# Performance work log

Hardware: AMD Instinct MI355X
Metric: run time of the kernel (lower is better)

## Reference

```python
import jax, jax.numpy as jnp
import numpy as np

C = 256
LN_EPS = 1e-5
LEAKY_SLOPE = 0.01

def _layernorm(t, g, b):
    mu = jnp.mean(t, axis=-1, keepdims=True)
    var = jnp.mean((t - mu) ** 2, axis=-1, keepdims=True)
    return (t - mu) * jax.lax.rsqrt(var + LN_EPS) * g + b

def setup_inputs() -> dict:
    key = jax.random.key(0)
    ks = jax.random.split(key, 16)
    b, d, h, w = 4, 4096, 64, 64
    s = lambda n: 1.0 / np.sqrt(n)
    return {
        "x": jax.random.normal(ks[0], (b, 1, d), jnp.float32),
        "y": jax.random.normal(ks[1], (b, C, h, w), jnp.float32),
        "q_w": jax.random.normal(ks[2], (C, C), jnp.float32) * s(C),
        "q_b": jnp.zeros((C,), jnp.float32),
        "dw_w": jax.random.normal(ks[3], (C,), jnp.float32),
        "dw_b": jnp.zeros((C,), jnp.float32),
        "kv_w1": jax.random.normal(ks[4], (1, C // 2), jnp.float32),
        "kv_b1": jnp.zeros((C // 2,), jnp.float32),
        "ln1_g": jnp.ones((C // 2,), jnp.float32),
        "ln1_b": jnp.zeros((C // 2,), jnp.float32),
        "kv_w2": jax.random.normal(ks[5], (C // 2, C), jnp.float32) * s(C // 2),
        "kv_b2": jnp.zeros((C,), jnp.float32),
        "ln2_g": jnp.ones((C,), jnp.float32),
        "ln2_b": jnp.zeros((C,), jnp.float32),
        "kv_w3": jax.random.normal(ks[6], (C, C), jnp.float32) * s(C),
        "kv_b3": jnp.zeros((C,), jnp.float32),
        "ln3_g": jnp.ones((C,), jnp.float32),
        "ln3_b": jnp.zeros((C,), jnp.float32),
        "kv_w4": jax.random.normal(ks[7], (C, 2 * C), jnp.float32) * s(C),
        "kv_b4": jnp.zeros((2 * C,), jnp.float32),
        "proj_w": jax.random.normal(ks[8], (C, C), jnp.float32) * s(C),
        "proj_b": jnp.zeros((C,), jnp.float32),
    }

def reference(x, y, q_w, q_b, dw_w, dw_b, kv_w1, kv_b1, ln1_g, ln1_b,
              kv_w2, kv_b2, ln2_g, ln2_b, kv_w3, kv_b3, ln3_g, ln3_b,
              kv_w4, kv_b4, proj_w, proj_b):
    b, c, h, w = y.shape
    # x: [b, 1, d] -> [b, d, 1]; MLP kv-generator lifts each scalar to 2c channels
    t = jnp.swapaxes(x, 1, 2)  # [b, d, 1]
    t = jax.nn.leaky_relu(_layernorm(t @ kv_w1 + kv_b1, ln1_g, ln1_b), LEAKY_SLOPE)
    t = jax.nn.leaky_relu(_layernorm(t @ kv_w2 + kv_b2, ln2_g, ln2_b), LEAKY_SLOPE)
    t = jax.nn.leaky_relu(_layernorm(t @ kv_w3 + kv_b3, ln3_g, ln3_b), LEAKY_SLOPE)
    t = jax.nn.silu(t @ kv_w4 + kv_b4)  # [b, d, 2c]
    k, v = jnp.split(t, 2, axis=-1)  # each [b, d, c]
    k = jnp.swapaxes(k, 1, 2)  # [b, c, d]
    # q = dwconv1x1(conv1x1(y)): 1x1 conv is a channel matmul; depthwise 1x1 is per-channel affine
    q = jnp.einsum('bchw,oc->bohw', y, q_w) + q_b[None, :, None, None]
    q = q * dw_w[None, :, None, None] + dw_b[None, :, None, None]
    q = q.reshape(b, c, h * w).transpose(0, 2, 1)  # [b, hw, c]
    scores = jnp.einsum('bic,bcd->bid', q, k) * (float(c) ** -0.5)  # [b, hw, d]
    attn = jax.nn.softmax(scores, axis=2)
    h_ = jnp.einsum('bid,bdc->bic', attn, v)  # [b, hw, c]
    h_ = h_.transpose(0, 2, 1).reshape(b, c, h, w)
    h_ = jnp.einsum('bchw,oc->bohw', h_, proj_w) + proj_b[None, :, None, None]
    return y + h_
```

## Files before the change

kernel.cpp:

```cpp
#include <hip/hip_runtime.h>
#include <cstdint>
#include <cstddef>

using bf16   = __bf16;
using bf16x8 = __bf16 __attribute__((ext_vector_type(8)));
using f32x4  = float  __attribute__((ext_vector_type(4)));
using u16    = unsigned short;
using ushort8 = __attribute__((ext_vector_type(8))) unsigned short;

#define MFMA16(a, b, c) __builtin_amdgcn_mfma_f32_16x16x32_bf16(a, b, c, 0, 0, 0)

__device__ __forceinline__ u16 f2bf(float f) {
  union { float f; unsigned u; } v; v.f = f;
  unsigned r = v.u + 0x7fffu + ((v.u >> 16) & 1u);
  return (u16)(r >> 16);
}
__device__ __forceinline__ u16 bfc(float f) {
  union { float f; unsigned u; } v; v.f = f;
  return (u16)((v.u + 0x8000u) >> 16);
}
__device__ __forceinline__ float b2f(u16 h) {
  union { unsigned u; float f; } v; v.u = ((unsigned)h) << 16; return v.f;
}
__device__ __forceinline__ bf16x8 ldb8(const u16* p) { return *(const bf16x8*)p; }
__device__ __forceinline__ float red_sum16(float v) {
  v += __shfl_xor(v, 1, 64); v += __shfl_xor(v, 2, 64);
  v += __shfl_xor(v, 4, 64); v += __shfl_xor(v, 8, 64);
  return v;
}
__device__ __forceinline__ void gll16(const u16* g, u16* l) {
  __builtin_amdgcn_global_load_lds(
      (const __attribute__((address_space(1))) void*)g,
      (__attribute__((address_space(3))) void*)l, 16, 0, 0);
}

#define QSCALE 0.09016844005556021f

__global__ void k_prep(const float* __restrict__ kv_w2, const float* __restrict__ kv_w3,
                       const float* __restrict__ kv_w4, const float* __restrict__ q_w,
                       const float* __restrict__ proj_w,
                       u16* __restrict__ Wt2, u16* __restrict__ Wt3, u16* __restrict__ Wt4,
                       u16* __restrict__ Qw, u16* __restrict__ Pww) {
  int idx = blockIdx.x * 256 + threadIdx.x;
  if (idx < 32768) {
    int n = idx >> 7, k = idx & 127;
    Wt2[idx] = f2bf(kv_w2[k * 256 + n]);
  } else if (idx < 98304) {
    int j = idx - 32768, n = j >> 8, k = j & 255;
    Wt3[j] = f2bf(kv_w3[k * 256 + n]);
  } else if (idx < 229376) {
    int j = idx - 98304, n = j >> 8, k = j & 255;
    Wt4[j] = f2bf(kv_w4[k * 512 + n]);
  } else if (idx < 294912) {
    int j = idx - 229376;
    Qw[j] = f2bf(q_w[j]);
  } else if (idx < 360448) {
    int j = idx - 294912;
    Pww[j] = f2bf(proj_w[j]);
  }
}

__device__ __forceinline__ void ln_store(f32x4* acc, const float* __restrict__ bias,
    const float* __restrict__ g, const float* __restrict__ bb, u16* act,
    int w, int quad, int l16) {
  #pragma unroll
  for (int f = 0; f < 16; ++f) {
    float bv = bias[f * 16 + l16];
    acc[f][0] += bv; acc[f][1] += bv; acc[f][2] += bv; acc[f][3] += bv;
  }
  #pragma unroll
  for (int r = 0; r < 4; ++r) {
    float s = 0;
    #pragma unroll
    for (int f = 0; f < 16; ++f) s += acc[f][r];
    s = red_sum16(s);
    float mu = s * (1.f / 256.f);
    float vv = 0;
    #pragma unroll
    for (int f = 0; f < 16; ++f) { float d = acc[f][r] - mu; vv += d * d; }
    vv = red_sum16(vv);
    float inv = rsqrtf(vv * (1.f / 256.f) + 1e-5f);
    int rl = w * 16 + quad * 4 + r;
    #pragma unroll
    for (int f = 0; f < 16; ++f) {
      int col = f * 16 + l16;
      float o = (acc[f][r] - mu) * inv * g[col] + bb[col];
      o = o > 0.f ? o : 0.01f * o;
      act[rl * 264 + col] = f2bf(o);
    }
  }
}

template<int K>
__device__ __forceinline__ void mlp_layer(u16* act, u16* sW, const u16* __restrict__ Wt,
    const float* __restrict__ bias, const float* __restrict__ g, const float* __restrict__ bb,
    int tid, int w, int quad, int l16) {
  bf16x8 af[K / 32];
  #pragma unroll
  for (int kk = 0; kk < K / 32; ++kk) af[kk] = ldb8(act + (w * 16 + l16) * 264 + kk * 32 + quad * 8);
  f32x4 z = {0.f, 0.f, 0.f, 0.f};
  f32x4 acc[16];
  #pragma unroll
  for (int f = 0; f < 16; ++f) acc[f] = z;
  for (int nc = 0; nc < 8; ++nc) {
    __syncthreads();
    #pragma unroll
    for (int p = 0; p < K / 64; ++p) {
      int q = p * 256 + tid; int row = q / (K / 8), c8 = q % (K / 8);
      *(uint4*)(sW + row * 264 + c8 * 8) = *(const uint4*)(Wt + (size_t)(nc * 32 + row) * K + c8 * 8);
    }
    __syncthreads();
    #pragma unroll
    for (int nb = 0; nb < 2; ++nb) {
      int f = nc * 2 + nb;
      #pragma unroll
      for (int kk = 0; kk < K / 32; ++kk)
        acc[f] = MFMA16(af[kk], ldb8(sW + (nb * 16 + l16) * 264 + kk * 32 + quad * 8), acc[f]);
    }
  }
  ln_store(acc, bias, g, bb, act, w, quad, l16);
  __syncthreads();
}

__device__ __forceinline__ void mlp_layer4(u16* act, u16* sW, const u16* __restrict__ Wt4,
    const float* __restrict__ bias4, u16* __restrict__ Kt, u16* __restrict__ Vt,
    int i0, int tid, int w, int quad, int l16) {
  bf16x8 af[8];
  #pragma unroll
  for (int kk = 0; kk < 8; ++kk) af[kk] = ldb8(act + (w * 16 + l16) * 264 + kk * 32 + quad * 8);
  f32x4 z = {0.f, 0.f, 0.f, 0.f};
  for (int h = 0; h < 2; ++h) {
    f32x4 acc[16];
    #pragma unroll
    for (int f = 0; f < 16; ++f) acc[f] = z;
    for (int nc = 0; nc < 8; ++nc) {
      __syncthreads();
      #pragma unroll
      for (int p = 0; p < 4; ++p) {
        int q = p * 256 + tid; int row = q >> 5, c8 = q & 31;
        *(uint4*)(sW + row * 264 + c8 * 8) =
            *(const uint4*)(Wt4 + (size_t)(h * 256 + nc * 32 + row) * 256 + c8 * 8);
      }
      __syncthreads();
      #pragma unroll
      for (int nb = 0; nb < 2; ++nb) {
        int f = nc * 2 + nb;
        #pragma unroll
        for (int kk = 0; kk < 8; ++kk)
          acc[f] = MFMA16(af[kk], ldb8(sW + (nb * 16 + l16) * 264 + kk * 32 + quad * 8), acc[f]);
      }
    }
    #pragma unroll
    for (int f = 0; f < 16; ++f) {
      int col = f * 16 + l16;
      float bv = bias4[h * 256 + col];
      if (h == 0) {
        int kk = f >> 1;
        int qs = (f & 1) * 2 + (l16 >> 3);
        int e  = l16 & 7;
        int l16base = (w & 1) * 8 + quad * 2;
        size_t tb = ((size_t)((i0 >> 5) + (w >> 1))) * 8192 + kk * 1024 + qs * 128 + e;
        #pragma unroll
        for (int r = 0; r < 4; ++r) {
          float v = acc[f][r] + bv;
          v = v / (1.f + __expf(-v));
          Kt[tb + (size_t)(r & 1) * 512 + (size_t)(l16base + (r >> 1)) * 8] = f2bf(v);
        }
      } else {
        int rowg0 = i0 + w * 16 + quad * 4;
        int bb2 = rowg0 >> 12;
        int tt = (rowg0 >> 5) & 127;
        int qv = (rowg0 >> 3) & 3;
        int e0 = rowg0 & 7;
        ushort4 u;
        #pragma unroll
        for (int r = 0; r < 4; ++r) {
          float v = acc[f][r] + bv;
          v = v / (1.f + __expf(-v));
          ((u16*)&u)[r] = f2bf(v);
        }
        size_t off = ((size_t)(bb2 * 128 + tt)) * 8192 + f * 512 + qv * 128 + l16 * 8 + e0;
        *(ushort4*)(Vt + off) = u;
      }
    }
  }
}

__global__ __launch_bounds__(256, 2) void k_fused(
    const float* __restrict__ x, const float* __restrict__ w1, const float* __restrict__ bias1,
    const float* __restrict__ g1, const float* __restrict__ bb1,
    const u16* __restrict__ Wt2, const float* __restrict__ bias2,
    const float* __restrict__ g2, const float* __restrict__ bb2,
    const u16* __restrict__ Wt3, const float* __restrict__ bias3,
    const float* __restrict__ g3, const float* __restrict__ bb3,
    const u16* __restrict__ Wt4, const float* __restrict__ bias4,
    const float* __restrict__ y, const u16* __restrict__ Qw,
    const float* __restrict__ qb, const float* __restrict__ dww, const float* __restrict__ dwb,
    u16* __restrict__ Kt, u16* __restrict__ Vt, u16* __restrict__ Qb) {
  __shared__ __align__(16) u16 smem[25344];
  int tid = threadIdx.x, w = tid >> 6, lane = tid & 63, quad = lane >> 4, l16 = lane & 15;

  if (blockIdx.x < 256) {
    u16* act = smem;
    u16* sW  = smem + 16896;
    int i0 = blockIdx.x * 64;
    {
      int rloc = w * 16 + (lane >> 2);
      int c0 = (lane & 3) * 32;
      float xv = x[i0 + rloc];
      float t[32];
      float s = 0.f;
      #pragma unroll
      for (int j = 0; j < 32; ++j) { t[j] = xv * w1[c0 + j] + bias1[c0 + j]; s += t[j]; }
      s += __shfl_xor(s, 1, 64); s += __shfl_xor(s, 2, 64);
      float mu = s * (1.f / 128.f);
      float vv = 0.f;
      #pragma unroll
      for (int j = 0; j < 32; ++j) { float d = t[j] - mu; vv += d * d; }
      vv += __shfl_xor(vv, 1, 64); vv += __shfl_xor(vv, 2, 64);
      float inv = rsqrtf(vv * (1.f / 128.f) + 1e-5f);
      #pragma unroll
      for (int jo = 0; jo < 4; ++jo) {
        ushort8 pk;
        #pragma unroll
        for (int e = 0; e < 8; ++e) {
          int j = jo * 8 + e;
          float o = (t[j] - mu) * inv * g1[c0 + j] + bb1[c0 + j];
          o = o > 0.f ? o : 0.01f * o;
          pk[e] = f2bf(o);
        }
        *(ushort8*)(act + rloc * 264 + c0 + jo * 8) = pk;
      }
    }
    __syncthreads();
    mlp_layer<128>(act, sW, Wt2, bias2, g2, bb2, tid, w, quad, l16);
    mlp_layer<256>(act, sW, Wt3, bias3, g3, bb3, tid, w, quad, l16);
    mlp_layer4(act, sW, Wt4, bias4, Kt, Vt, i0, tid, w, quad, l16);
    return;
  }

  u16* sY = smem;
  u16* sB = smem + 4608;
  int t = blockIdx.x - 256;
  int b = t >> 6, i0 = (t & 63) * 64;
  f32x4 z = {0.f, 0.f, 0.f, 0.f};
  f32x4 acc[16];
  #pragma unroll
  for (int f = 0; f < 16; ++f) acc[f] = z;
  for (int kc = 0; kc < 4; ++kc) {
    if (kc) __syncthreads();
    {
      int cl = tid >> 4;
      int il = (tid & 15) * 4;
      #pragma unroll
      for (int p = 0; p < 4; ++p) {
        int c = kc * 64 + p * 16 + cl;
        float4 v = *(const float4*)(y + ((size_t)(b * 256 + c)) * 4096 + i0 + il);
        sY[(il + 0) * 72 + p * 16 + cl] = f2bf(v.x);
        sY[(il + 1) * 72 + p * 16 + cl] = f2bf(v.y);
        sY[(il + 2) * 72 + p * 16 + cl] = f2bf(v.z);
        sY[(il + 3) * 72 + p * 16 + cl] = f2bf(v.w);
      }
    }
    #pragma unroll
    for (int p = 0; p < 8; ++p) {
      int q = p * 256 + tid; int row = q >> 3, k8 = q & 7;
      *(uint4*)(sB + row * 72 + k8 * 8) = *(const uint4*)(Qw + (size_t)row * 256 + kc * 64 + k8 * 8);
    }
    __syncthreads();
    #pragma unroll
    for (int kk = 0; kk < 2; ++kk) {
      bf16x8 af = ldb8(sY + (w * 16 + l16) * 72 + kk * 32 + quad * 8);
      #pragma unroll
      for (int f = 0; f < 16; ++f) {
        bf16x8 bfr = ldb8(sB + (f * 16 + l16) * 72 + kk * 32 + quad * 8);
        acc[f] = MFMA16(af, bfr, acc[f]);
      }
    }
  }
  #pragma unroll
  for (int f = 0; f < 16; ++f) {
    int col = f * 16 + l16;
    float q0 = qb[col], sc = dww[col], dB = dwb[col];
    #pragma unroll
    for (int r = 0; r < 4; ++r) {
      int rowg = i0 + w * 16 + quad * 4 + r;
      float v = ((acc[f][r] + q0) * sc + dB) * QSCALE;
      Qb[((size_t)(b * 4096 + rowg)) * 256 + col] = f2bf(v);
    }
  }
}

__global__ __launch_bounds__(256, 2) void k_attn(const u16* __restrict__ Qb, const u16* __restrict__ Kt,
    const u16* __restrict__ Vt, u16* __restrict__ Op, float* __restrict__ Ol) {
  __shared__ __align__(16) u16 smem[37888];
  int tid = threadIdx.x, w = tid >> 6, lane = tid & 63, quad = lane >> 4, l16 = lane & 15;
  int b = blockIdx.x & 3, kh = (blockIdx.x >> 2) & 3, qt = blockIdx.x >> 4;
  int i0 = qt * 128 + w * 32;

  bf16x8 qf[2][8];
  {
    const u16* qrow = Qb + ((size_t)(b * 4096 + i0 + l16)) * 256 + quad * 8;
    #pragma unroll
    for (int kk = 0; kk < 8; ++kk) {
      qf[0][kk] = ldb8(qrow + kk * 32);
      qf[1][kk] = ldb8(qrow + 16 * 256 + kk * 32);
    }
  }
  f32x4 z = {0.f, 0.f, 0.f, 0.f};
  f32x4 oacc[2][16];
  #pragma unroll
  for (int sub = 0; sub < 2; ++sub)
    #pragma unroll
    for (int f = 0; f < 16; ++f) oacc[sub][f] = z;
  float l4[2][4] = {{0.f, 0.f, 0.f, 0.f}, {0.f, 0.f, 0.f, 0.f}};

  u16* sPw = smem + 32768 + w * 1280;
  int wp = w & 1;
  const u16* gSrc = ((w < 2) ? Kt : Vt) + ((size_t)(b * 128 + kh * 32) * 8192) + wp * 4096 + lane * 8;
  u16* lBase = smem + ((w < 2) ? 0 : 8192) + wp * 4096 + lane * 8;

  #pragma unroll
  for (int i = 0; i < 8; ++i) gll16(gSrc + i * 512, lBase + i * 512);
  gSrc += 8192;

  #pragma unroll 1
  for (int kt = 0; kt < 32; ++kt) {
    int buf = kt & 1;
    const u16* sK = smem + buf * 16384;
    const u16* sV = sK + 8192;
    asm volatile("s_waitcnt vmcnt(0)" ::: "memory");
    __syncthreads();
    if (kt < 31) {
      u16* dst = lBase + (buf ^ 1) * 16384;
      #pragma unroll
      for (int i = 0; i < 8; ++i) gll16(gSrc + i * 512, dst + i * 512);
      gSrc += 8192;
    }
    f32x4 s00 = z, s01 = z, s10 = z, s11 = z;
    const u16* kb = sK + lane * 8;
    __builtin_amdgcn_s_setprio(1);
    #pragma unroll
    for (int kk = 0; kk < 8; ++kk) {
      bf16x8 k0 = ldb8(kb + kk * 1024);
      bf16x8 k1 = ldb8(kb + kk * 1024 + 512);
      s00 = MFMA16(qf[0][kk], k0, s00);
      s01 = MFMA16(qf[0][kk], k1, s01);
      s10 = MFMA16(qf[1][kk], k0, s10);
      s11 = MFMA16(qf[1][kk], k1, s11);
    }
    __builtin_amdgcn_s_setprio(0);
    #pragma unroll
    for (int r = 0; r < 4; ++r) {
      float p0 = exp2f(s00[r]);
      float p1 = exp2f(s01[r]);
      float p2 = exp2f(s10[r]);
      float p3 = exp2f(s11[r]);
      l4[0][r] += p0 + p1;
      l4[1][r] += p2 + p3;
      unsigned pk0 = ((unsigned)bfc(p1) << 16) | (unsigned)bfc(p0);
      unsigned pk1 = ((unsigned)bfc(p3) << 16) | (unsigned)bfc(p2);
      int row0 = (quad * 4 + r) * 40;
      *(unsigned*)(sPw + row0 + l16 * 2) = pk0;
      *(unsigned*)(sPw + 640 + row0 + l16 * 2) = pk1;
    }
    asm volatile("s_waitcnt lgkmcnt(0)" ::: "memory");
    bf16x8 pf0 = ldb8(sPw + l16 * 40 + quad * 8);
    bf16x8 pf1 = ldb8(sPw + 640 + l16 * 40 + quad * 8);
    const u16* vbase = sV + lane * 8;
    __builtin_amdgcn_s_setprio(1);
    #pragma unroll
    for (int f = 0; f < 16; ++f) {
      bf16x8 vf = ldb8(vbase + f * 512);
      oacc[0][f] = MFMA16(pf0, vf, oacc[0][f]);
      oacc[1][f] = MFMA16(pf1, vf, oacc[1][f]);
    }
    __builtin_amdgcn_s_setprio(0);
  }
  #pragma unroll
  for (int sub = 0; sub < 2; ++sub)
    #pragma unroll
    for (int r = 0; r < 4; ++r) l4[sub][r] = red_sum16(l4[sub][r]);
  #pragma unroll
  for (int sub = 0; sub < 2; ++sub)
    #pragma unroll
    for (int r = 0; r < 4; ++r) {
      size_t gr = (size_t)kh * 16384 + b * 4096 + i0 + sub * 16 + quad * 4 + r;
      u16* orow = Op + gr * 256;
      #pragma unroll
      for (int f = 0; f < 16; ++f) orow[f * 16 + l16] = f2bf(oacc[sub][f][r]);
      if (l16 == 0) Ol[gr] = l4[sub][r];
    }
}

__global__ __launch_bounds__(256) void k_proj(const u16* __restrict__ Op, const float* __restrict__ Ol,
    const u16* __restrict__ Pw, const float* __restrict__ pb, const float* __restrict__ y,
    float* __restrict__ out) {
  __shared__ __align__(16) u16 sA[128 * 136];
  __shared__ __align__(16) u16 sB[64 * 136];
  __shared__ float sW[64];
  int tid = threadIdx.x, w = tid >> 6, lane = tid & 63, quad = lane >> 4, l16 = lane & 15;
  int i0 = blockIdx.x * 64, o0 = blockIdx.y * 128, b = blockIdx.z;
  if (tid < 64) {
    size_t gr = (size_t)b * 4096 + i0 + tid;
    float L = Ol[gr] + Ol[gr + 16384] + Ol[gr + 32768] + Ol[gr + 49152];
    sW[tid] = 1.f / L;
  }
  __syncthreads();
  f32x4 z = {0.f, 0.f, 0.f, 0.f};
  f32x4 acc[2][4] = {{z, z, z, z}, {z, z, z, z}};
  for (int kc = 0; kc < 2; ++kc) {
    if (kc) __syncthreads();
    #pragma unroll
    for (int p = 0; p < 8; ++p) {
      int q = p * 256 + tid; int row = q >> 4, c8 = q & 15;
      *(uint4*)(sA + row * 136 + c8 * 8) = *(const uint4*)(Pw + ((size_t)(o0 + row)) * 256 + kc * 128 + c8 * 8);
    }
    #pragma unroll
    for (int p = 0; p < 4; ++p) {
      int q = p * 256 + tid; int row = q >> 4, c8 = q & 15;
      size_t gr = (size_t)b * 4096 + i0 + row;
      const u16* hp = Op + gr * 256 + kc * 128 + c8 * 8;
      uint4 u0 = *(const uint4*)(hp);
      uint4 u1 = *(const uint4*)(hp + 4194304);
      uint4 u2 = *(const uint4*)(hp + 8388608);
      uint4 u3 = *(const uint4*)(hp + 12582912);
      float wr = sW[row];
      const u16* p0 = (const u16*)&u0; const u16* p1 = (const u16*)&u1;
      const u16* p2 = (const u16*)&u2; const u16* p3 = (const u16*)&u3;
      ushort8 ov;
      #pragma unroll
      for (int e = 0; e < 8; ++e) {
        float v = (b2f(p0[e]) + b2f(p1[e]) + b2f(p2[e]) + b2f(p3[e])) * wr;
        ov[e] = f2bf(v);
      }
      *(ushort8*)(sB + row * 136 + c8 * 8) = ov;
    }
    __syncthreads();
    #pragma unroll
    for (int kk = 0; kk < 4; ++kk) {
      bf16x8 af0 = ldb8(sA + (w * 16 + l16) * 136 + kk * 32 + quad * 8);
      bf16x8 af1 = ldb8(sA + (64 + w * 16 + l16) * 136 + kk * 32 + quad * 8);
      #pragma unroll
      for (int nb = 0; nb < 4; ++nb) {
        bf16x8 bfr = ldb8(sB + (nb * 16 + l16) * 136 + kk * 32 + quad * 8);
        acc[0][nb] = MFMA16(af0, bfr, acc[0][nb]);
        acc[1][nb] = MFMA16(af1, bfr, acc[1][nb]);
      }
    }
  }
  #pragma unroll
  for (int oc = 0; oc < 2; ++oc)
    #pragma unroll
    for (int nb = 0; nb < 4; ++nb)
      #pragma unroll
      for (int r = 0; r < 4; ++r) {
        int og = o0 + oc * 64 + w * 16 + quad * 4 + r;
        size_t idx = ((size_t)(b * 256 + og)) * 4096 + i0 + nb * 16 + l16;
        out[idx] = y[idx] + acc[oc][nb][r] + pb[og];
      }
}

extern "C" void kernel_launch(void* const* d_in, const int* in_sizes, int n_in,
                              void* d_out, int out_size, void* d_ws, size_t ws_size,
                              hipStream_t stream) {
  (void)in_sizes; (void)n_in; (void)out_size; (void)ws_size;
  const float* x     = (const float*)d_in[0];
  const float* y     = (const float*)d_in[1];
  const float* q_w   = (const float*)d_in[2];
  const float* q_b   = (const float*)d_in[3];
  const float* dw_w  = (const float*)d_in[4];
  const float* dw_b  = (const float*)d_in[5];
  const float* kv_w1 = (const float*)d_in[6];
  const float* kv_b1 = (const float*)d_in[7];
  const float* ln1_g = (const float*)d_in[8];
  const float* ln1_b = (const float*)d_in[9];
  const float* kv_w2 = (const float*)d_in[10];
  const float* kv_b2 = (const float*)d_in[11];
  const float* ln2_g = (const float*)d_in[12];
  const float* ln2_b = (const float*)d_in[13];
  const float* kv_w3 = (const float*)d_in[14];
  const float* kv_b3 = (const float*)d_in[15];
  const float* ln3_g = (const float*)d_in[16];
  const float* ln3_b = (const float*)d_in[17];
  const float* kv_w4 = (const float*)d_in[18];
  const float* kv_b4 = (const float*)d_in[19];
  const float* proj_w = (const float*)d_in[20];
  const float* proj_b = (const float*)d_in[21];
  float* out = (float*)d_out;
  unsigned char* ws = (unsigned char*)d_ws;

  u16* Wt2 = (u16*)(ws + 0);
  u16* Wt3 = (u16*)(ws + 65536);
  u16* Wt4 = (u16*)(ws + 196608);
  u16* Qw  = (u16*)(ws + 458752);
  u16* Pww = (u16*)(ws + 589824);
  u16* Qb  = (u16*)(ws + 9437184);
  u16* Kt  = (u16*)(ws + 17825792);
  u16* Vt  = (u16*)(ws + 26214400);
  u16* Op  = (u16*)(ws + 34603008);
  float* Ol = (float*)(ws + 68157440);

  k_prep<<<1408, 256, 0, stream>>>(kv_w2, kv_w3, kv_w4, q_w, proj_w, Wt2, Wt3, Wt4, Qw, Pww);
  k_fused<<<512, 256, 0, stream>>>(x, kv_w1, kv_b1, ln1_g, ln1_b,
                                   Wt2, kv_b2, ln2_g, ln2_b,
                                   Wt3, kv_b3, ln3_g, ln3_b,
                                   Wt4, kv_b4,
                                   y, Qw, q_b, dw_w, dw_b,
                                   Kt, Vt, Qb);
  k_attn<<<512, 256, 0, stream>>>(Qb, Kt, Vt, Op, Ol);
  k_proj<<<dim3(64, 2, 4), 256, 0, stream>>>(Op, Ol, Pww, proj_b, y, out);
}
```

Measured before the change: 236.8 us.

## Split attention work across 8 waves with 16 query rows each

```diff
diff --git a/kernel.cpp b/kernel.cpp
--- a/kernel.cpp
+++ b/kernel.cpp
@@ -291,37 +291,32 @@
   }
 }
 
-__global__ __launch_bounds__(256, 2) void k_attn(const u16* __restrict__ Qb, const u16* __restrict__ Kt,
+__global__ __launch_bounds__(512, 4) void k_attn(const u16* __restrict__ Qb, const u16* __restrict__ Kt,
     const u16* __restrict__ Vt, u16* __restrict__ Op, float* __restrict__ Ol) {
   __shared__ __align__(16) u16 smem[37888];
   int tid = threadIdx.x, w = tid >> 6, lane = tid & 63, quad = lane >> 4, l16 = lane & 15;
   int b = blockIdx.x & 3, kh = (blockIdx.x >> 2) & 3, qt = blockIdx.x >> 4;
-  int i0 = qt * 128 + w * 32;
-
-  bf16x8 qf[2][8];
+  int i0 = qt * 128 + w * 16;
+
+  bf16x8 qf[8];
   {
     const u16* qrow = Qb + ((size_t)(b * 4096 + i0 + l16)) * 256 + quad * 8;
     #pragma unroll
-    for (int kk = 0; kk < 8; ++kk) {
-      qf[0][kk] = ldb8(qrow + kk * 32);
-      qf[1][kk] = ldb8(qrow + 16 * 256 + kk * 32);
-    }
+    for (int kk = 0; kk < 8; ++kk) qf[kk] = ldb8(qrow + kk * 32);
   }
   f32x4 z = {0.f, 0.f, 0.f, 0.f};
-  f32x4 oacc[2][16];
-  #pragma unroll
-  for (int sub = 0; sub < 2; ++sub)
-    #pragma unroll
-    for (int f = 0; f < 16; ++f) oacc[sub][f] = z;
-  float l4[2][4] = {{0.f, 0.f, 0.f, 0.f}, {0.f, 0.f, 0.f, 0.f}};
-
-  u16* sPw = smem + 32768 + w * 1280;
-  int wp = w & 1;
-  const u16* gSrc = ((w < 2) ? Kt : Vt) + ((size_t)(b * 128 + kh * 32) * 8192) + wp * 4096 + lane * 8;
-  u16* lBase = smem + ((w < 2) ? 0 : 8192) + wp * 4096 + lane * 8;
-
-  #pragma unroll
-  for (int i = 0; i < 8; ++i) gll16(gSrc + i * 512, lBase + i * 512);
+  f32x4 oacc[16];
+  #pragma unroll
+  for (int f = 0; f < 16; ++f) oacc[f] = z;
+  float l4[4] = {0.f, 0.f, 0.f, 0.f};
+
+  u16* sPw = smem + 32768 + w * 640;
+  int wq = w & 3;
+  const u16* gSrc = ((w < 4) ? Kt : Vt) + ((size_t)(b * 128 + kh * 32) * 8192) + wq * 2048 + lane * 8;
+  u16* lBase = smem + ((w < 4) ? 0 : 8192) + wq * 2048 + lane * 8;
+
+  #pragma unroll
+  for (int i = 0; i < 4; ++i) gll16(gSrc + i * 512, lBase + i * 512);
   gSrc += 8192;
 
   #pragma unroll 1
@@ -334,63 +329,50 @@
     if (kt < 31) {
       u16* dst = lBase + (buf ^ 1) * 16384;
       #pragma unroll
-      for (int i = 0; i < 8; ++i) gll16(gSrc + i * 512, dst + i * 512);
+      for (int i = 0; i < 4; ++i) gll16(gSrc + i * 512, dst + i * 512);
       gSrc += 8192;
     }
-    f32x4 s00 = z, s01 = z, s10 = z, s11 = z;
+    f32x4 s00 = z, s01 = z;
     const u16* kb = sK + lane * 8;
     __builtin_amdgcn_s_setprio(1);
     #pragma unroll
     for (int kk = 0; kk < 8; ++kk) {
       bf16x8 k0 = ldb8(kb + kk * 1024);
       bf16x8 k1 = ldb8(kb + kk * 1024 + 512);
-      s00 = MFMA16(qf[0][kk], k0, s00);
-      s01 = MFMA16(qf[0][kk], k1, s01);
-      s10 = MFMA16(qf[1][kk], k0, s10);
-      s11 = MFMA16(qf[1][kk], k1, s11);
+      s00 = MFMA16(qf[kk], k0, s00);
+      s01 = MFMA16(qf[kk], k1, s01);
     }
     __builtin_amdgcn_s_setprio(0);
     #pragma unroll
     for (int r = 0; r < 4; ++r) {
       float p0 = exp2f(s00[r]);
       float p1 = exp2f(s01[r]);
-      float p2 = exp2f(s10[r]);
-      float p3 = exp2f(s11[r]);
-      l4[0][r] += p0 + p1;
-      l4[1][r] += p2 + p3;
+      l4[r] += p0 + p1;
       unsigned pk0 = ((unsigned)bfc(p1) << 16) | (unsigned)bfc(p0);
-      unsigned pk1 = ((unsigned)bfc(p3) << 16) | (unsigned)bfc(p2);
       int row0 = (quad * 4 + r) * 40;
       *(unsigned*)(sPw + row0 + l16 * 2) = pk0;
-      *(unsigned*)(sPw + 640 + row0 + l16 * 2) = pk1;
     }
     asm volatile("s_waitcnt lgkmcnt(0)" ::: "memory");
     bf16x8 pf0 = ldb8(sPw + l16 * 40 + quad * 8);
-    bf16x8 pf1 = ldb8(sPw + 640 + l16 * 40 + quad * 8);
     const u16* vbase = sV + lane * 8;
     __builtin_amdgcn_s_setprio(1);
     #pragma unroll
     for (int f = 0; f < 16; ++f) {
       bf16x8 vf = ldb8(vbase + f * 512);
-      oacc[0][f] = MFMA16(pf0, vf, oacc[0][f]);
-      oacc[1][f] = MFMA16(pf1, vf, oacc[1][f]);
+      oacc[f] = MFMA16(pf0, vf, oacc[f]);
     }
     __builtin_amdgcn_s_setprio(0);
   }
   #pragma unroll
-  for (int sub = 0; sub < 2; ++sub)
-    #pragma unroll
-    for (int r = 0; r < 4; ++r) l4[sub][r] = red_sum16(l4[sub][r]);
-  #pragma unroll
-  for (int sub = 0; sub < 2; ++sub)
-    #pragma unroll
-    for (int r = 0; r < 4; ++r) {
-      size_t gr = (size_t)kh * 16384 + b * 4096 + i0 + sub * 16 + quad * 4 + r;
-      u16* orow = Op + gr * 256;
-      #pragma unroll
-      for (int f = 0; f < 16; ++f) orow[f * 16 + l16] = f2bf(oacc[sub][f][r]);
-      if (l16 == 0) Ol[gr] = l4[sub][r];
-    }
+  for (int r = 0; r < 4; ++r) l4[r] = red_sum16(l4[r]);
+  #pragma unroll
+  for (int r = 0; r < 4; ++r) {
+    size_t gr = (size_t)kh * 16384 + b * 4096 + i0 + quad * 4 + r;
+    u16* orow = Op + gr * 256;
+    #pragma unroll
+    for (int f = 0; f < 16; ++f) orow[f * 16 + l16] = f2bf(oacc[f][r]);
+    if (l16 == 0) Ol[gr] = l4[r];
+  }
 }
 
 __global__ __launch_bounds__(256) void k_proj(const u16* __restrict__ Op, const float* __restrict__ Ol,
@@ -508,6 +490,6 @@
                                    Wt4, kv_b4,
                                    y, Qw, q_b, dw_w, dw_b,
                                    Kt, Vt, Qb);
-  k_attn<<<512, 256, 0, stream>>>(Qb, Kt, Vt, Op, Ol);
+  k_attn<<<512, 512, 0, stream>>>(Qb, Kt, Vt, Op, Ol);
   k_proj<<<dim3(64, 2, 4), 256, 0, stream>>>(Op, Ol, Pww, proj_b, y, out);
 }
```

Result: no change. 238.8 us (+0.8%).

## Software-pipeline attention loop: compute next QK scores after current PV

Applied to the files above, without the earlier changes.

```diff
diff --git a/kernel.cpp b/kernel.cpp
--- a/kernel.cpp
+++ b/kernel.cpp
@@ -317,28 +317,28 @@
 
   u16* sPw = smem + 32768 + w * 1280;
   int wp = w & 1;
-  const u16* gSrc = ((w < 2) ? Kt : Vt) + ((size_t)(b * 128 + kh * 32) * 8192) + wp * 4096 + lane * 8;
-  u16* lBase = smem + ((w < 2) ? 0 : 8192) + wp * 4096 + lane * 8;
-
-  #pragma unroll
-  for (int i = 0; i < 8; ++i) gll16(gSrc + i * 512, lBase + i * 512);
-  gSrc += 8192;
-
-  #pragma unroll 1
-  for (int kt = 0; kt < 32; ++kt) {
-    int buf = kt & 1;
-    const u16* sK = smem + buf * 16384;
-    const u16* sV = sK + 8192;
-    asm volatile("s_waitcnt vmcnt(0)" ::: "memory");
-    __syncthreads();
-    if (kt < 31) {
-      u16* dst = lBase + (buf ^ 1) * 16384;
-      #pragma unroll
-      for (int i = 0; i < 8; ++i) gll16(gSrc + i * 512, dst + i * 512);
-      gSrc += 8192;
-    }
+  size_t tb = (size_t)(b * 128 + kh * 32) * 8192;
+  const u16* gK = Kt + tb + wp * 4096 + lane * 8;
+  const u16* gV = Vt + tb + wp * 4096 + lane * 8;
+  u16* lK0 = smem + wp * 4096 + lane * 8;
+  u16* lK1 = smem + 8192 + wp * 4096 + lane * 8;
+  u16* lV0 = smem + 16384 + wp * 4096 + lane * 8;
+  u16* lV1 = smem + 24576 + wp * 4096 + lane * 8;
+
+  if (w < 2) {
+    #pragma unroll
+    for (int i = 0; i < 8; ++i) gll16(gK + i * 512, lK0 + i * 512);
+    #pragma unroll
+    for (int i = 0; i < 8; ++i) gll16(gK + 8192 + i * 512, lK1 + i * 512);
+  } else {
+    #pragma unroll
+    for (int i = 0; i < 8; ++i) gll16(gV + i * 512, lV0 + i * 512);
+  }
+  asm volatile("s_waitcnt vmcnt(0)" ::: "memory");
+  __syncthreads();
+  {
     f32x4 s00 = z, s01 = z, s10 = z, s11 = z;
-    const u16* kb = sK + lane * 8;
+    const u16* kb = smem + lane * 8;
     __builtin_amdgcn_s_setprio(1);
     #pragma unroll
     for (int kk = 0; kk < 8; ++kk) {
@@ -364,6 +364,29 @@
       *(unsigned*)(sPw + row0 + l16 * 2) = pk0;
       *(unsigned*)(sPw + 640 + row0 + l16 * 2) = pk1;
     }
+  }
+  asm volatile("s_waitcnt lgkmcnt(0)" ::: "memory");
+  __syncthreads();
+
+  #pragma unroll 1
+  for (int j = 0; j < 32; ++j) {
+    const u16* sK = smem + ((j + 1) & 1) * 8192;
+    const u16* sV = smem + 16384 + (j & 1) * 8192;
+    if (w < 2) {
+      if (j < 30) {
+        u16* dst = (j & 1) ? lK1 : lK0;
+        const u16* src = gK + (size_t)(j + 2) * 8192;
+        #pragma unroll
+        for (int i = 0; i < 8; ++i) gll16(src + i * 512, dst + i * 512);
+      }
+    } else {
+      if (j < 31) {
+        u16* dst = ((j + 1) & 1) ? lV1 : lV0;
+        const u16* src = gV + (size_t)(j + 1) * 8192;
+        #pragma unroll
+        for (int i = 0; i < 8; ++i) gll16(src + i * 512, dst + i * 512);
+      }
+    }
     asm volatile("s_waitcnt lgkmcnt(0)" ::: "memory");
     bf16x8 pf0 = ldb8(sPw + l16 * 40 + quad * 8);
     bf16x8 pf1 = ldb8(sPw + 640 + l16 * 40 + quad * 8);
@@ -376,6 +399,37 @@
       oacc[1][f] = MFMA16(pf1, vf, oacc[1][f]);
     }
     __builtin_amdgcn_s_setprio(0);
+    if (j < 31) {
+      f32x4 s00 = z, s01 = z, s10 = z, s11 = z;
+      const u16* kb = sK + lane * 8;
+      __builtin_amdgcn_s_setprio(1);
+      #pragma unroll
+      for (int kk = 0; kk < 8; ++kk) {
+        bf16x8 k0 = ldb8(kb + kk * 1024);
+        bf16x8 k1 = ldb8(kb + kk * 1024 + 512);
+        s00 = MFMA16(qf[0][kk], k0, s00);
+        s01 = MFMA16(qf[0][kk], k1, s01);
+        s10 = MFMA16(qf[1][kk], k0, s10);
+        s11 = MFMA16(qf[1][kk], k1, s11);
+      }
+      __builtin_amdgcn_s_setprio(0);
+      #pragma unroll
+      for (int r = 0; r < 4; ++r) {
+        float p0 = exp2f(s00[r]);
+        float p1 = exp2f(s01[r]);
+        float p2 = exp2f(s10[r]);
+        float p3 = exp2f(s11[r]);
+        l4[0][r] += p0 + p1;
+        l4[1][r] += p2 + p3;
+        unsigned pk0 = ((unsigned)bfc(p1) << 16) | (unsigned)bfc(p0);
+        unsigned pk1 = ((unsigned)bfc(p3) << 16) | (unsigned)bfc(p2);
+        int row0 = (quad * 4 + r) * 40;
+        *(unsigned*)(sPw + row0 + l16 * 2) = pk0;
+        *(unsigned*)(sPw + 640 + row0 + l16 * 2) = pk1;
+      }
+      asm volatile("s_waitcnt vmcnt(0)" ::: "memory");
+      __syncthreads();
+    }
   }
   #pragma unroll
   for (int sub = 0; sub < 2; ++sub)
```

Result: no change. 238.3 us (+0.6%).

## Pre-swizzle weights into MFMA fragment order and load B operands from global

Applied to the files above, without the earlier changes.

```diff
diff --git a/kernel.cpp b/kernel.cpp
--- a/kernel.cpp
+++ b/kernel.cpp
@@ -43,17 +43,21 @@
                        u16* __restrict__ Qw, u16* __restrict__ Pww) {
   int idx = blockIdx.x * 256 + threadIdx.x;
   if (idx < 32768) {
-    int n = idx >> 7, k = idx & 127;
-    Wt2[idx] = f2bf(kv_w2[k * 256 + n]);
+    int j = idx, e = j & 7, l = (j >> 3) & 63, t = j >> 9;
+    int kk = t & 3, f = t >> 2;
+    Wt2[j] = f2bf(kv_w2[(kk * 32 + (l >> 4) * 8 + e) * 256 + f * 16 + (l & 15)]);
   } else if (idx < 98304) {
-    int j = idx - 32768, n = j >> 8, k = j & 255;
-    Wt3[j] = f2bf(kv_w3[k * 256 + n]);
+    int j = idx - 32768, e = j & 7, l = (j >> 3) & 63, t = j >> 9;
+    int kk = t & 7, f = t >> 3;
+    Wt3[j] = f2bf(kv_w3[(kk * 32 + (l >> 4) * 8 + e) * 256 + f * 16 + (l & 15)]);
   } else if (idx < 229376) {
-    int j = idx - 98304, n = j >> 8, k = j & 255;
-    Wt4[j] = f2bf(kv_w4[k * 512 + n]);
+    int j = idx - 98304, e = j & 7, l = (j >> 3) & 63, t = j >> 9;
+    int kk = t & 7, f4 = t >> 3;
+    Wt4[j] = f2bf(kv_w4[(kk * 32 + (l >> 4) * 8 + e) * 512 + f4 * 16 + (l & 15)]);
   } else if (idx < 294912) {
-    int j = idx - 229376;
-    Qw[j] = f2bf(q_w[j]);
+    int j = idx - 229376, e = j & 7, l = (j >> 3) & 63, t = j >> 9;
+    int k8 = t & 7, f = t >> 3;
+    Qw[j] = f2bf(q_w[(f * 16 + (l & 15)) * 256 + k8 * 32 + (l >> 4) * 8 + e]);
   } else if (idx < 360448) {
     int j = idx - 294912;
     Pww[j] = f2bf(proj_w[j]);
@@ -91,64 +95,42 @@
   }
 }
 
-template<int K>
-__device__ __forceinline__ void mlp_layer(u16* act, u16* sW, const u16* __restrict__ Wt,
+template<int KK>
+__device__ __forceinline__ void mlp_layer_g(u16* act, const u16* __restrict__ Wf,
     const float* __restrict__ bias, const float* __restrict__ g, const float* __restrict__ bb,
-    int tid, int w, int quad, int l16) {
-  bf16x8 af[K / 32];
-  #pragma unroll
-  for (int kk = 0; kk < K / 32; ++kk) af[kk] = ldb8(act + (w * 16 + l16) * 264 + kk * 32 + quad * 8);
+    int lane, int w, int quad, int l16) {
+  bf16x8 af[KK];
+  #pragma unroll
+  for (int kk = 0; kk < KK; ++kk) af[kk] = ldb8(act + (w * 16 + l16) * 264 + kk * 32 + quad * 8);
   f32x4 z = {0.f, 0.f, 0.f, 0.f};
   f32x4 acc[16];
-  #pragma unroll
-  for (int f = 0; f < 16; ++f) acc[f] = z;
-  for (int nc = 0; nc < 8; ++nc) {
-    __syncthreads();
-    #pragma unroll
-    for (int p = 0; p < K / 64; ++p) {
-      int q = p * 256 + tid; int row = q / (K / 8), c8 = q % (K / 8);
-      *(uint4*)(sW + row * 264 + c8 * 8) = *(const uint4*)(Wt + (size_t)(nc * 32 + row) * K + c8 * 8);
-    }
-    __syncthreads();
-    #pragma unroll
-    for (int nb = 0; nb < 2; ++nb) {
-      int f = nc * 2 + nb;
-      #pragma unroll
-      for (int kk = 0; kk < K / 32; ++kk)
-        acc[f] = MFMA16(af[kk], ldb8(sW + (nb * 16 + l16) * 264 + kk * 32 + quad * 8), acc[f]);
-    }
+  const u16* bp = Wf + (size_t)lane * 8;
+  #pragma unroll
+  for (int f = 0; f < 16; ++f) {
+    acc[f] = z;
+    #pragma unroll
+    for (int kk = 0; kk < KK; ++kk)
+      acc[f] = MFMA16(af[kk], ldb8(bp + (size_t)(f * KK + kk) * 512), acc[f]);
   }
   ln_store(acc, bias, g, bb, act, w, quad, l16);
-  __syncthreads();
-}
-
-__device__ __forceinline__ void mlp_layer4(u16* act, u16* sW, const u16* __restrict__ Wt4,
+}
+
+__device__ __forceinline__ void mlp_layer4_g(u16* act, const u16* __restrict__ Wf4,
     const float* __restrict__ bias4, u16* __restrict__ Kt, u16* __restrict__ Vt,
-    int i0, int tid, int w, int quad, int l16) {
+    int i0, int lane, int w, int quad, int l16) {
   bf16x8 af[8];
   #pragma unroll
   for (int kk = 0; kk < 8; ++kk) af[kk] = ldb8(act + (w * 16 + l16) * 264 + kk * 32 + quad * 8);
   f32x4 z = {0.f, 0.f, 0.f, 0.f};
+  const u16* bp = Wf4 + (size_t)lane * 8;
   for (int h = 0; h < 2; ++h) {
     f32x4 acc[16];
     #pragma unroll
-    for (int f = 0; f < 16; ++f) acc[f] = z;
-    for (int nc = 0; nc < 8; ++nc) {
-      __syncthreads();
-      #pragma unroll
-      for (int p = 0; p < 4; ++p) {
-        int q = p * 256 + tid; int row = q >> 5, c8 = q & 31;
-        *(uint4*)(sW + row * 264 + c8 * 8) =
-            *(const uint4*)(Wt4 + (size_t)(h * 256 + nc * 32 + row) * 256 + c8 * 8);
-      }
-      __syncthreads();
-      #pragma unroll
-      for (int nb = 0; nb < 2; ++nb) {
-        int f = nc * 2 + nb;
-        #pragma unroll
-        for (int kk = 0; kk < 8; ++kk)
-          acc[f] = MFMA16(af[kk], ldb8(sW + (nb * 16 + l16) * 264 + kk * 32 + quad * 8), acc[f]);
-      }
+    for (int f = 0; f < 16; ++f) {
+      acc[f] = z;
+      #pragma unroll
+      for (int kk = 0; kk < 8; ++kk)
+        acc[f] = MFMA16(af[kk], ldb8(bp + (size_t)((h * 16 + f) * 8 + kk) * 512), acc[f]);
     }
     #pragma unroll
     for (int f = 0; f < 16; ++f) {
@@ -197,12 +179,11 @@
     const float* __restrict__ y, const u16* __restrict__ Qw,
     const float* __restrict__ qb, const float* __restrict__ dww, const float* __restrict__ dwb,
     u16* __restrict__ Kt, u16* __restrict__ Vt, u16* __restrict__ Qb) {
-  __shared__ __align__(16) u16 smem[25344];
+  __shared__ __align__(16) u16 smem[16896];
   int tid = threadIdx.x, w = tid >> 6, lane = tid & 63, quad = lane >> 4, l16 = lane & 15;
 
   if (blockIdx.x < 256) {
     u16* act = smem;
-    u16* sW  = smem + 16896;
     int i0 = blockIdx.x * 64;
     {
       int rloc = w * 16 + (lane >> 2);
@@ -232,21 +213,20 @@
         *(ushort8*)(act + rloc * 264 + c0 + jo * 8) = pk;
       }
     }
-    __syncthreads();
-    mlp_layer<128>(act, sW, Wt2, bias2, g2, bb2, tid, w, quad, l16);
-    mlp_layer<256>(act, sW, Wt3, bias3, g3, bb3, tid, w, quad, l16);
-    mlp_layer4(act, sW, Wt4, bias4, Kt, Vt, i0, tid, w, quad, l16);
+    mlp_layer_g<4>(act, Wt2, bias2, g2, bb2, lane, w, quad, l16);
+    mlp_layer_g<8>(act, Wt3, bias3, g3, bb3, lane, w, quad, l16);
+    mlp_layer4_g(act, Wt4, bias4, Kt, Vt, i0, lane, w, quad, l16);
     return;
   }
 
   u16* sY = smem;
-  u16* sB = smem + 4608;
   int t = blockIdx.x - 256;
   int b = t >> 6, i0 = (t & 63) * 64;
   f32x4 z = {0.f, 0.f, 0.f, 0.f};
   f32x4 acc[16];
   #pragma unroll
   for (int f = 0; f < 16; ++f) acc[f] = z;
+  const u16* qbp = Qw + (size_t)lane * 8;
   for (int kc = 0; kc < 4; ++kc) {
     if (kc) __syncthreads();
     {
@@ -262,18 +242,13 @@
         sY[(il + 3) * 72 + p * 16 + cl] = f2bf(v.w);
       }
     }
-    #pragma unroll
-    for (int p = 0; p < 8; ++p) {
-      int q = p * 256 + tid; int row = q >> 3, k8 = q & 7;
-      *(uint4*)(sB + row * 72 + k8 * 8) = *(const uint4*)(Qw + (size_t)row * 256 + kc * 64 + k8 * 8);
-    }
     __syncthreads();
     #pragma unroll
     for (int kk = 0; kk < 2; ++kk) {
       bf16x8 af = ldb8(sY + (w * 16 + l16) * 72 + kk * 32 + quad * 8);
       #pragma unroll
       for (int f = 0; f < 16; ++f) {
-        bf16x8 bfr = ldb8(sB + (f * 16 + l16) * 72 + kk * 32 + quad * 8);
+        bf16x8 bfr = ldb8(qbp + (size_t)(f * 8 + kc * 2 + kk) * 512);
         acc[f] = MFMA16(af, bfr, acc[f]);
       }
     }
```

Measured after the change: 288.9 us. 1.22x slower.
